# Kernel optimization log

Hardware: AMD Instinct MI355X
Metric: run time of the kernel (lower is better)

## Reference

```python
import jax, jax.numpy as jnp
import numpy as np

EPS = 1e-5


def _binary_act(x):
    # Forward: sign(x). Backward: piecewise-polynomial surrogate (ApproxSign STE).
    out3 = jnp.where(x < -1, -1.0,
            jnp.where(x < 0, x * x + 2.0 * x,
             jnp.where(x < 1, -x * x + 2.0 * x, 1.0)))
    return jax.lax.stop_gradient(jnp.sign(x) - out3) + out3


def _binarize_weights(w):
    # Per-output-channel scaling factor (detached), forward = scale*sign(w),
    # backward flows through clamp(w, -1, 1) (STE).
    scale = jax.lax.stop_gradient(jnp.mean(jnp.abs(w), axis=(1, 2, 3), keepdims=True))
    clipped = jnp.clip(w, -1.0, 1.0)
    return jax.lax.stop_gradient(scale * jnp.sign(w) - clipped) + clipped


def setup_inputs() -> dict:
    key = jax.random.key(0)
    kx, kw = jax.random.split(key)
    B, Cin, Cout, H, W = 32, 128, 128, 56, 56
    x = jax.random.normal(kx, (B, Cin, H, W), dtype=jnp.float32)
    # HardBinaryConv: weight = rand(n)*0.001 permuted then reshaped -> just random in [0, 0.001)
    w = jax.random.uniform(kw, (Cout, Cin, 3, 3), dtype=jnp.float32) * 0.001
    return {
        "x": x,
        "bias0": jnp.zeros((Cin,), jnp.float32),   # move0 LearnableBias
        "w": w,                                     # HardBinaryConv latent weights
        "gamma": jnp.ones((Cout,), jnp.float32),    # BN weight
        "beta": jnp.zeros((Cout,), jnp.float32),    # BN bias
        "bias1": jnp.zeros((Cout,), jnp.float32),   # move1
        "alpha": jnp.full((Cout,), 0.25, jnp.float32),  # PReLU per-channel
        "bias2": jnp.zeros((Cout,), jnp.float32),   # move2
    }


def reference(x, bias0, w, gamma, beta, bias1, alpha, bias2):
    def pc(v):  # per-channel broadcast (1, C, 1, 1)
        return v[None, :, None, None]

    residual = x
    out = x + pc(bias0)                     # move0
    out = _binary_act(out)                  # binary activation
    bw = _binarize_weights(w)               # {-scale, +scale} weights
    y = jax.lax.conv_general_dilated(
        out, bw, window_strides=(1, 1), padding=((1, 1), (1, 1)),
        dimension_numbers=("NCHW", "OIHW", "NCHW"))
    # BatchNorm2d (training mode: biased batch statistics over N,H,W)
    mean = jnp.mean(y, axis=(0, 2, 3), keepdims=True)
    var = jnp.mean(jnp.square(y - mean), axis=(0, 2, 3), keepdims=True)
    y = (y - mean) * jax.lax.rsqrt(var + EPS) * pc(gamma) + pc(beta)
    y = y + residual
    y = y + pc(bias1)                       # move1
    y = jnp.where(y >= 0, y, pc(alpha) * y)  # PReLU
    y = y + pc(bias2)                       # move2
    return y
```

## Files before the change

### kernel.cpp

```cpp
#include <hip/hip_runtime.h>
#include <stdint.h>

#define NB 32
#define NC 128
#define NH 56
#define NW 56
#define NHW_ (NH * NW)
#define NPIX (NB * NHW_)
#define NO 128
#define NK 1152
#define NSTRIP 14
#define NSLOT (NB * NSTRIP)

typedef unsigned long long u64;

__global__ __launch_bounds__(256) void pack_act(const float* __restrict__ x,
                                                const float* __restrict__ bias0,
                                                u64* __restrict__ packA) {
    int p = blockIdx.x * 256 + threadIdx.x;
    if (p >= NPIX) return;
    int n = p / NHW_;
    int rem = p - n * NHW_;
    const float* xb = x + (size_t)n * NC * NHW_ + rem;
    u64 w0 = 0, w1 = 0;
#pragma unroll 8
    for (int c = 0; c < 64; ++c)
        w0 |= (u64)((xb[(size_t)c * NHW_] + bias0[c]) > 0.f) << c;
#pragma unroll 8
    for (int c = 0; c < 64; ++c)
        w1 |= (u64)((xb[(size_t)(c + 64) * NHW_] + bias0[c + 64]) > 0.f) << c;
    packA[(size_t)p * 2]     = w0;
    packA[(size_t)p * 2 + 1] = w1;
}

__global__ __launch_bounds__(64) void pack_wgt(const float* __restrict__ w,
                                               u64* __restrict__ packW,
                                               float* __restrict__ scaleW,
                                               int* __restrict__ corrW) {
    __shared__ u64 sb[18];
    int o = blockIdx.x;
    int t = threadIdx.x;
    const float* wo = w + (size_t)o * NK;
    float s = 0.f;
    for (int i = t; i < NK; i += 64) s += fabsf(wo[i]);
    for (int off = 32; off; off >>= 1) s += __shfl_down(s, off);
    if (t == 0) scaleW[o] = s / (float)NK;
    if (t < 18) {
        int tap = t >> 1;
        int j   = t & 1;
        u64 bits = 0;
        for (int cc = 0; cc < 64; ++cc) {
            int c = j * 64 + cc;
            bits |= (u64)(wo[c * 9 + tap] > 0.f) << cc;
        }
        packW[(size_t)o * 18 + t] = bits;
        sb[t] = bits;
    }
    __syncthreads();
    if (t == 0) {
        int cv[9];
#pragma unroll
        for (int tap = 0; tap < 9; ++tap)
            cv[tap] = NC - 2 * (__popcll(sb[2 * tap]) + __popcll(sb[2 * tap + 1]));
        int* cw = corrW + o * 8;
        cw[0] = cv[0] + cv[3] + cv[6];
        cw[1] = cv[2] + cv[5] + cv[8];
        cw[2] = cv[0] + cv[1] + cv[2];
        cw[3] = cv[6] + cv[7] + cv[8];
        cw[4] = cv[0];
        cw[5] = cv[2];
        cw[6] = cv[6];
        cw[7] = cv[8];
    }
}

__global__ __launch_bounds__(256, 3) void conv_bin(const u64* __restrict__ packA,
                                                   const u64* __restrict__ packW,
                                                   const int* __restrict__ corrW,
                                                   short* __restrict__ yI,
                                                   int* __restrict__ sumP,
                                                   int* __restrict__ sqP) {
    __shared__ u64 lw[32 * 18];
    __shared__ int lc[32 * 8];

    int bid = blockIdx.x;
    int n = bid / (NSTRIP * 4);
    int rem = bid - n * (NSTRIP * 4);
    int strip = rem >> 2;
    int cg = rem & 3;
    int obase = cg * 32;
    int h0 = strip * 4;

    for (int i = threadIdx.x; i < 32 * 18; i += 256) lw[i] = packW[(size_t)obase * 18 + i];
    if (threadIdx.x < 32 * 8) lc[threadIdx.x] = corrW[obase * 8 + threadIdx.x];

    int wv = threadIdx.x >> 6, lane = threadIdx.x & 63;
    bool act = lane < NW;
    bool top = (strip == 0), bot = (strip == NSTRIP - 1);

    u64 a[6][3][2];
    bool cvv[3];
    cvv[0] = act && (lane >= 1);
    cvv[1] = act;
    cvv[2] = act && (lane + 1 < NW);
#pragma unroll
    for (int r = 0; r < 6; ++r) {
        int hi = h0 - 1 + r;
        bool rvv = (hi >= 0) && (hi < NH);
        int hc = hi < 0 ? 0 : (hi >= NH ? NH - 1 : hi);
#pragma unroll
        for (int c = 0; c < 3; ++c) {
            int wi = lane - 1 + c;
            int wc = wi < 0 ? 0 : (wi >= NW ? NW - 1 : wi);
            ulonglong2 q = *reinterpret_cast<const ulonglong2*>(
                packA + ((size_t)n * NHW_ + (size_t)hc * NW + wc) * 2);
            bool v = rvv && cvv[c];
            a[r][c][0] = v ? q.x : 0;
            a[r][c][1] = v ? q.y : 0;
        }
    }
    __syncthreads();

    bool isL = (lane == 0), isR = (lane == NW - 1);
    short* ybase = yI + (size_t)n * NO * NHW_ + (size_t)h0 * NW + lane;
    int sl = n * NSTRIP + strip;

    for (int oo = 0; oo < 8; ++oo) {
        int lo = (wv << 3) + oo;
        int o = obase + lo;
        const u64* wp = &lw[lo * 18];
        int pc0 = 0, pc1 = 0, pc2 = 0, pc3 = 0;
#pragma unroll
        for (int kh = 0; kh < 3; ++kh) {
#pragma unroll
            for (int kw = 0; kw < 3; ++kw) {
                u64 w0 = wp[(kh * 3 + kw) * 2];
                u64 w1 = wp[(kh * 3 + kw) * 2 + 1];
                pc0 += __popcll(a[0 + kh][kw][0] ^ w0) + __popcll(a[0 + kh][kw][1] ^ w1);
                pc1 += __popcll(a[1 + kh][kw][0] ^ w0) + __popcll(a[1 + kh][kw][1] ^ w1);
                pc2 += __popcll(a[2 + kh][kw][0] ^ w0) + __popcll(a[2 + kh][kw][1] ^ w1);
                pc3 += __popcll(a[3 + kh][kw][0] ^ w0) + __popcll(a[3 + kh][kw][1] ^ w1);
            }
        }
        const int* cw = &lc[lo * 8];
        int corrcol = isL ? cw[0] : (isR ? cw[1] : 0);
        int base = NK - corrcol;
        int d0 = base - 2 * pc0;
        int d1 = base - 2 * pc1;
        int d2 = base - 2 * pc2;
        int d3 = base - 2 * pc3;
        if (top) d0 -= cw[2] - (isL ? cw[4] : (isR ? cw[5] : 0));
        if (bot) d3 -= cw[3] - (isL ? cw[6] : (isR ? cw[7] : 0));
        if (act) {
            short* yp = ybase + (size_t)o * NHW_;
            yp[0]      = (short)d0;
            yp[NW]     = (short)d1;
            yp[2 * NW] = (short)d2;
            yp[3 * NW] = (short)d3;
        }
        int s = act ? (d0 + d1 + d2 + d3) : 0;
        int q = act ? (d0 * d0 + d1 * d1 + d2 * d2 + d3 * d3) : 0;
#pragma unroll
        for (int off = 32; off; off >>= 1) {
            s += __shfl_down(s, off);
            q += __shfl_down(q, off);
        }
        if (lane == 0) {
            sumP[o * NSLOT + sl] = s;
            sqP[o * NSLOT + sl]  = q;
        }
    }
}

__global__ __launch_bounds__(64) void bn_coef2(const int* __restrict__ sumP,
                                               const int* __restrict__ sqP,
                                               const float* __restrict__ scaleW,
                                               const float* __restrict__ gamma,
                                               const float* __restrict__ beta,
                                               const float* __restrict__ bias1,
                                               float* __restrict__ coefA,
                                               float* __restrict__ coefB) {
    int o = blockIdx.x;
    int t = threadIdx.x;
    long long s = 0, q = 0;
    for (int i = t; i < NSLOT; i += 64) {
        s += sumP[o * NSLOT + i];
        q += sqP[o * NSLOT + i];
    }
#pragma unroll
    for (int off = 32; off; off >>= 1) {
        s += __shfl_down(s, off);
        q += __shfl_down(q, off);
    }
    if (t == 0) {
        double cnt = (double)NPIX;
        double mean = (double)s / cnt;
        double var = (double)q / cnt - mean * mean;
        if (var < 0.0) var = 0.0;
        float sc = scaleW[o];
        float rs = rsqrtf((float)((double)sc * (double)sc * var) + 1e-5f);
        float g = gamma[o];
        coefA[o] = sc * g * rs;
        coefB[o] = beta[o] - (float)((double)sc * mean) * g * rs + bias1[o];
    }
}

__global__ __launch_bounds__(256) void final_store(const short* __restrict__ yI,
                                                   const float* __restrict__ x,
                                                   const float* __restrict__ coefA,
                                                   const float* __restrict__ coefB,
                                                   const float* __restrict__ alpha,
                                                   const float* __restrict__ bias2,
                                                   float* __restrict__ out) {
    const size_t ngroups = (size_t)NB * NO * NHW_ / 8;
    for (size_t g = (size_t)blockIdx.x * blockDim.x + threadIdx.x; g < ngroups;
         g += (size_t)gridDim.x * blockDim.x) {
        size_t i = g * 8;
        int o = (int)((i / NHW_) % NO);
        float a = coefA[o], bb = coefB[o], al = alpha[o], b2 = bias2[o];
        int4 yv = *reinterpret_cast<const int4*>(yI + i);
        float4 x0 = *reinterpret_cast<const float4*>(x + i);
        float4 x1 = *reinterpret_cast<const float4*>(x + i + 4);
        int q[4] = {yv.x, yv.y, yv.z, yv.w};
        float xs[8] = {x0.x, x0.y, x0.z, x0.w, x1.x, x1.y, x1.z, x1.w};
        float r[8];
#pragma unroll
        for (int j = 0; j < 4; ++j) {
            float lo = (float)(short)(q[j] & 0xffff);
            float hi = (float)(q[j] >> 16);
            float t0 = fmaf(a, lo, bb) + xs[2 * j];
            float t1 = fmaf(a, hi, bb) + xs[2 * j + 1];
            t0 = t0 >= 0.f ? t0 : al * t0;
            t1 = t1 >= 0.f ? t1 : al * t1;
            r[2 * j]     = t0 + b2;
            r[2 * j + 1] = t1 + b2;
        }
        float4 o0 = {r[0], r[1], r[2], r[3]};
        float4 o1 = {r[4], r[5], r[6], r[7]};
        *reinterpret_cast<float4*>(out + i)     = o0;
        *reinterpret_cast<float4*>(out + i + 4) = o1;
    }
}

__device__ inline void load_nbhd(const u64* __restrict__ packA, int n, int h,
                                 int wcol, bool act, u64 a[9][2], unsigned* vmask) {
    unsigned m = 0;
#pragma unroll
    for (int kh = 0; kh < 3; ++kh) {
        int hi = h + kh - 1;
        bool vh = (hi >= 0) && (hi < NH);
#pragma unroll
        for (int kw = 0; kw < 3; ++kw) {
            int wi = wcol + kw - 1;
            int t = kh * 3 + kw;
            bool v = act && vh && (wi >= 0) && (wi < NW);
            int hc = hi < 0 ? 0 : (hi >= NH ? NH - 1 : hi);
            int wc = wi < 0 ? 0 : (wi >= NW ? NW - 1 : wi);
            size_t idx = ((size_t)n * NHW_ + (size_t)hc * NW + wc) * 2;
            u64 q0 = packA[idx], q1 = packA[idx + 1];
            a[t][0] = v ? q0 : 0;
            a[t][1] = v ? q1 : 0;
            m |= (unsigned)v << t;
        }
    }
    *vmask = m;
}

__global__ __launch_bounds__(256) void conv_stats_atomic(const u64* __restrict__ packA,
                                                         const u64* __restrict__ packW,
                                                         int* __restrict__ sumI,
                                                         u64* __restrict__ sumsqI) {
    __shared__ u64 lw[NO * 18];
    for (int i = threadIdx.x; i < NO * 18; i += 256) lw[i] = packW[i];
    int nh = blockIdx.x;
    int n = nh / NH, h = nh - n * NH;
    int wave = threadIdx.x >> 6, lane = threadIdx.x & 63;
    bool act = lane < NW;
    u64 a[9][2]; unsigned vm;
    load_nbhd(packA, n, h, lane, act, a, &vm);
    __syncthreads();
    for (int oo = 0; oo < 32; ++oo) {
        int o = (wave << 5) + oo;
        int dot = 0;
#pragma unroll
        for (int t = 0; t < 9; ++t) {
            int pc = __popcll(a[t][0] ^ lw[(o * 9 + t) * 2]) +
                     __popcll(a[t][1] ^ lw[(o * 9 + t) * 2 + 1]);
            dot += ((vm >> t) & 1) ? (NC - 2 * pc) : 0;
        }
        int s = dot, sq = dot * dot;
        for (int off = 32; off; off >>= 1) {
            s  += __shfl_down(s, off);
            sq += __shfl_down(sq, off);
        }
        if (lane == 0) {
            atomicAdd(&sumI[o], s);
            atomicAdd(&sumsqI[o], (u64)(unsigned)sq);
        }
    }
}

__global__ __launch_bounds__(128) void bn_coef(const int* __restrict__ sumP,
                                               const u64* __restrict__ sqP,
                                               const float* __restrict__ scaleW,
                                               const float* __restrict__ gamma,
                                               const float* __restrict__ beta,
                                               const float* __restrict__ bias1,
                                               float* __restrict__ coefA,
                                               float* __restrict__ coefB) {
    int o = threadIdx.x;
    double cnt = (double)NPIX;
    double mean = (double)sumP[o] / cnt;
    double var = (double)sqP[o] / cnt - mean * mean;
    if (var < 0.0) var = 0.0;
    float sc = scaleW[o];
    float rs = rsqrtf((float)((double)sc * (double)sc * var) + 1e-5f);
    float g = gamma[o];
    coefA[o] = sc * g * rs;
    coefB[o] = beta[o] - (float)((double)sc * mean) * g * rs + bias1[o];
}

__global__ __launch_bounds__(256) void final_recompute(const u64* __restrict__ packA,
                                                       const u64* __restrict__ packW,
                                                       const float* __restrict__ coefA,
                                                       const float* __restrict__ coefB,
                                                       const float* __restrict__ alpha,
                                                       const float* __restrict__ bias2,
                                                       const float* __restrict__ x,
                                                       float* __restrict__ out) {
    __shared__ u64 lw[NO * 18];
    for (int i = threadIdx.x; i < NO * 18; i += 256) lw[i] = packW[i];
    int nh = blockIdx.x;
    int n = nh / NH, h = nh - n * NH;
    int wave = threadIdx.x >> 6, lane = threadIdx.x & 63;
    bool act = lane < NW;
    u64 a[9][2]; unsigned vm;
    load_nbhd(packA, n, h, lane, act, a, &vm);
    __syncthreads();
    for (int oo = 0; oo < 32; ++oo) {
        int o = (wave << 5) + oo;
        int dot = 0;
#pragma unroll
        for (int t = 0; t < 9; ++t) {
            int pc = __popcll(a[t][0] ^ lw[(o * 9 + t) * 2]) +
                     __popcll(a[t][1] ^ lw[(o * 9 + t) * 2 + 1]);
            dot += ((vm >> t) & 1) ? (NC - 2 * pc) : 0;
        }
        if (act) {
            size_t idx = ((size_t)n * NO + o) * NHW_ + (size_t)h * NW + lane;
            float t = fmaf(coefA[o], (float)dot, coefB[o]) + x[idx];
            t = t >= 0.f ? t : alpha[o] * t;
            out[idx] = t + bias2[o];
        }
    }
}

extern "C" void kernel_launch(void* const* d_in, const int* in_sizes, int n_in,
                              void* d_out, int out_size, void* d_ws, size_t ws_size,
                              hipStream_t stream) {
    (void)in_sizes; (void)n_in; (void)out_size;
    const float* x     = (const float*)d_in[0];
    const float* bias0 = (const float*)d_in[1];
    const float* w     = (const float*)d_in[2];
    const float* gamma = (const float*)d_in[3];
    const float* beta  = (const float*)d_in[4];
    const float* bias1 = (const float*)d_in[5];
    const float* alpha = (const float*)d_in[6];
    const float* bias2 = (const float*)d_in[7];
    float* out = (float*)d_out;
    char* ws = (char*)d_ws;

    u64*   packA  = (u64*)ws;
    u64*   packW  = (u64*)(ws + 1605632);
    int*   corrW  = (int*)(ws + 1624064);
    float* scaleW = (float*)(ws + 1628160);
    float* coefA  = (float*)(ws + 1628672);
    float* coefB  = (float*)(ws + 1629184);
    int*   sumI   = (int*)(ws + 1629696);
    u64*   sqI    = (u64*)(ws + 1630208);
    int*   sumP   = (int*)(ws + 1631232);
    int*   sqP    = (int*)(ws + 1860608);
    short* yI     = (short*)(ws + 2089984);
    bool store = ws_size >= (size_t)2089984 + (size_t)NB * NO * NHW_ * 2;

    pack_act<<<NPIX / 256, 256, 0, stream>>>(x, bias0, packA);
    pack_wgt<<<NO, 64, 0, stream>>>(w, packW, scaleW, corrW);

    if (store) {
        conv_bin<<<NB * NSTRIP * 4, 256, 0, stream>>>(packA, packW, corrW, yI, sumP, sqP);
        bn_coef2<<<NO, 64, 0, stream>>>(sumP, sqP, scaleW, gamma, beta, bias1, coefA, coefB);
        final_store<<<2048, 256, 0, stream>>>(yI, x, coefA, coefB, alpha, bias2, out);
    } else {
        hipMemsetAsync(sumI, 0, 512 + 1024, stream);
        conv_stats_atomic<<<NB * NH, 256, 0, stream>>>(packA, packW, sumI, sqI);
        bn_coef<<<1, NO, 0, stream>>>(sumI, sqI, scaleW, gamma, beta, bias1, coefA, coefB);
        final_recompute<<<NB * NH, 256, 0, stream>>>(packA, packW, coefA, coefB, alpha, bias2, x, out);
    }
}
```

Before: 93.34 us.

## Use zero-padded packed activations and halve conv block size

Packed activations are written into a zero-padded buffer (58x66 per image), so the conv kernel loads its neighbourhood without clamping or validity masks. The conv kernel now runs 128-thread blocks, each wave handling 16 output channels instead of 8. The recompute fallback is rebuilt as a templated conv_bin variant. This removes branch and select work in the load phase, at the cost of an extra memset of the padded buffer and slightly more pack_act writes.

```diff
diff --git a/kernel.cpp b/kernel.cpp
--- a/kernel.cpp
+++ b/kernel.cpp
@@ -12,15 +12,24 @@
 #define NSTRIP 14
 #define NSLOT (NB * NSTRIP)
 
+#define PADH 58
+#define PADW 66
+#define PAD_BYTES ((size_t)NB * PADH * PADW * 2 * 8)
+
 typedef unsigned long long u64;
+
+__device__ __forceinline__ size_t pidx(int n, int h, int w) {
+    return (((size_t)n * PADH + (h + 1)) * PADW + (w + 1)) * 2;
+}
 
 __global__ __launch_bounds__(256) void pack_act(const float* __restrict__ x,
                                                 const float* __restrict__ bias0,
-                                                u64* __restrict__ packA) {
+                                                u64* __restrict__ packAp) {
     int p = blockIdx.x * 256 + threadIdx.x;
     if (p >= NPIX) return;
     int n = p / NHW_;
     int rem = p - n * NHW_;
+    int h = rem / NW, wcol = rem - h * NW;
     const float* xb = x + (size_t)n * NC * NHW_ + rem;
     u64 w0 = 0, w1 = 0;
 #pragma unroll 8
@@ -29,8 +38,9 @@
 #pragma unroll 8
     for (int c = 0; c < 64; ++c)
         w1 |= (u64)((xb[(size_t)(c + 64) * NHW_] + bias0[c + 64]) > 0.f) << c;
-    packA[(size_t)p * 2]     = w0;
-    packA[(size_t)p * 2 + 1] = w1;
+    size_t idx = pidx(n, h, wcol);
+    packAp[idx]     = w0;
+    packAp[idx + 1] = w1;
 }
 
 __global__ __launch_bounds__(64) void pack_wgt(const float* __restrict__ w,
@@ -74,12 +84,14 @@
     }
 }
 
-__global__ __launch_bounds__(256, 3) void conv_bin(const u64* __restrict__ packA,
-                                                   const u64* __restrict__ packW,
-                                                   const int* __restrict__ corrW,
-                                                   short* __restrict__ yI,
-                                                   int* __restrict__ sumP,
-                                                   int* __restrict__ sqP) {
+template <int MODE>
+__global__ __launch_bounds__(128, 4) void conv_bin(
+    const u64* __restrict__ packAp, const u64* __restrict__ packW,
+    const int* __restrict__ corrW, short* __restrict__ yI,
+    int* __restrict__ sumP, int* __restrict__ sqP,
+    const float* __restrict__ coefA, const float* __restrict__ coefB,
+    const float* __restrict__ alpha, const float* __restrict__ bias2,
+    const float* __restrict__ x, float* __restrict__ out) {
     __shared__ u64 lw[32 * 18];
     __shared__ int lc[32 * 8];
 
@@ -87,60 +99,51 @@
     int n = bid / (NSTRIP * 4);
     int rem = bid - n * (NSTRIP * 4);
     int strip = rem >> 2;
-    int cg = rem & 3;
-    int obase = cg * 32;
+    int cgp = rem & 3;
+    int obase = cgp * 32;
     int h0 = strip * 4;
 
-    for (int i = threadIdx.x; i < 32 * 18; i += 256) lw[i] = packW[(size_t)obase * 18 + i];
-    if (threadIdx.x < 32 * 8) lc[threadIdx.x] = corrW[obase * 8 + threadIdx.x];
+    for (int i = threadIdx.x; i < 32 * 18; i += 128) lw[i] = packW[(size_t)obase * 18 + i];
+    for (int i = threadIdx.x; i < 32 * 8; i += 128) lc[i] = corrW[obase * 8 + i];
 
     int wv = threadIdx.x >> 6, lane = threadIdx.x & 63;
     bool act = lane < NW;
+
+    u64 a[6][3][2];
+    const u64* bp = packAp + (((size_t)n * PADH + h0) * PADW + lane) * 2;
+#pragma unroll
+    for (int r = 0; r < 6; ++r)
+#pragma unroll
+        for (int c = 0; c < 3; ++c) {
+            ulonglong2 q = *reinterpret_cast<const ulonglong2*>(bp + ((size_t)r * PADW + c) * 2);
+            a[r][c][0] = q.x;
+            a[r][c][1] = q.y;
+        }
+#pragma unroll
+    for (int r = 0; r < 6; ++r)
+#pragma unroll
+        for (int c = 0; c < 3; ++c)
+            asm volatile("" : "+v"(a[r][c][0]), "+v"(a[r][c][1]));
+    __syncthreads();
+
     bool top = (strip == 0), bot = (strip == NSTRIP - 1);
-
-    u64 a[6][3][2];
-    bool cvv[3];
-    cvv[0] = act && (lane >= 1);
-    cvv[1] = act;
-    cvv[2] = act && (lane + 1 < NW);
-#pragma unroll
-    for (int r = 0; r < 6; ++r) {
-        int hi = h0 - 1 + r;
-        bool rvv = (hi >= 0) && (hi < NH);
-        int hc = hi < 0 ? 0 : (hi >= NH ? NH - 1 : hi);
-#pragma unroll
-        for (int c = 0; c < 3; ++c) {
-            int wi = lane - 1 + c;
-            int wc = wi < 0 ? 0 : (wi >= NW ? NW - 1 : wi);
-            ulonglong2 q = *reinterpret_cast<const ulonglong2*>(
-                packA + ((size_t)n * NHW_ + (size_t)hc * NW + wc) * 2);
-            bool v = rvv && cvv[c];
-            a[r][c][0] = v ? q.x : 0;
-            a[r][c][1] = v ? q.y : 0;
-        }
-    }
-    __syncthreads();
-
     bool isL = (lane == 0), isR = (lane == NW - 1);
+    int sl = n * NSTRIP + strip;
     short* ybase = yI + (size_t)n * NO * NHW_ + (size_t)h0 * NW + lane;
-    int sl = n * NSTRIP + strip;
-
-    for (int oo = 0; oo < 8; ++oo) {
-        int lo = (wv << 3) + oo;
+
+    for (int oo = 0; oo < 16; ++oo) {
+        int lo = (wv << 4) + oo;
         int o = obase + lo;
         const u64* wp = &lw[lo * 18];
         int pc0 = 0, pc1 = 0, pc2 = 0, pc3 = 0;
 #pragma unroll
-        for (int kh = 0; kh < 3; ++kh) {
-#pragma unroll
-            for (int kw = 0; kw < 3; ++kw) {
-                u64 w0 = wp[(kh * 3 + kw) * 2];
-                u64 w1 = wp[(kh * 3 + kw) * 2 + 1];
-                pc0 += __popcll(a[0 + kh][kw][0] ^ w0) + __popcll(a[0 + kh][kw][1] ^ w1);
-                pc1 += __popcll(a[1 + kh][kw][0] ^ w0) + __popcll(a[1 + kh][kw][1] ^ w1);
-                pc2 += __popcll(a[2 + kh][kw][0] ^ w0) + __popcll(a[2 + kh][kw][1] ^ w1);
-                pc3 += __popcll(a[3 + kh][kw][0] ^ w0) + __popcll(a[3 + kh][kw][1] ^ w1);
-            }
+        for (int t = 0; t < 9; ++t) {
+            const int kh = t / 3, kw = t - 3 * (t / 3);
+            u64 w0 = wp[2 * t], w1 = wp[2 * t + 1];
+            pc0 += __popcll(a[kh][kw][0] ^ w0) + __popcll(a[kh][kw][1] ^ w1);
+            pc1 += __popcll(a[kh + 1][kw][0] ^ w0) + __popcll(a[kh + 1][kw][1] ^ w1);
+            pc2 += __popcll(a[kh + 2][kw][0] ^ w0) + __popcll(a[kh + 2][kw][1] ^ w1);
+            pc3 += __popcll(a[kh + 3][kw][0] ^ w0) + __popcll(a[kh + 3][kw][1] ^ w1);
         }
         const int* cw = &lc[lo * 8];
         int corrcol = isL ? cw[0] : (isR ? cw[1] : 0);
@@ -151,23 +154,38 @@
         int d3 = base - 2 * pc3;
         if (top) d0 -= cw[2] - (isL ? cw[4] : (isR ? cw[5] : 0));
         if (bot) d3 -= cw[3] - (isL ? cw[6] : (isR ? cw[7] : 0));
-        if (act) {
+
+        if (MODE == 0 && act) {
             short* yp = ybase + (size_t)o * NHW_;
             yp[0]      = (short)d0;
             yp[NW]     = (short)d1;
             yp[2 * NW] = (short)d2;
             yp[3 * NW] = (short)d3;
         }
-        int s = act ? (d0 + d1 + d2 + d3) : 0;
-        int q = act ? (d0 * d0 + d1 * d1 + d2 * d2 + d3 * d3) : 0;
-#pragma unroll
-        for (int off = 32; off; off >>= 1) {
-            s += __shfl_down(s, off);
-            q += __shfl_down(q, off);
-        }
-        if (lane == 0) {
-            sumP[o * NSLOT + sl] = s;
-            sqP[o * NSLOT + sl]  = q;
+        if (MODE <= 1) {
+            int s = act ? (d0 + d1 + d2 + d3) : 0;
+            int q = act ? (__mul24(d0, d0) + __mul24(d1, d1) +
+                           __mul24(d2, d2) + __mul24(d3, d3)) : 0;
+#pragma unroll
+            for (int off = 32; off; off >>= 1) {
+                s += __shfl_down(s, off);
+                q += __shfl_down(q, off);
+            }
+            if (lane == 0) {
+                sumP[o * NSLOT + sl] = s;
+                sqP[o * NSLOT + sl]  = q;
+            }
+        }
+        if (MODE == 2 && act) {
+            float ca = coefA[o], cb = coefB[o], al = alpha[o], b2 = bias2[o];
+            size_t idx = ((size_t)n * NO + o) * NHW_ + (size_t)h0 * NW + lane;
+            int dv[4] = {d0, d1, d2, d3};
+#pragma unroll
+            for (int r = 0; r < 4; ++r) {
+                float tv = fmaf(ca, (float)dv[r], cb) + x[idx + (size_t)r * NW];
+                tv = tv >= 0.f ? tv : al * tv;
+                out[idx + (size_t)r * NW] = tv + b2;
+            }
         }
     }
 }
@@ -242,119 +260,6 @@
     }
 }
 
-__device__ inline void load_nbhd(const u64* __restrict__ packA, int n, int h,
-                                 int wcol, bool act, u64 a[9][2], unsigned* vmask) {
-    unsigned m = 0;
-#pragma unroll
-    for (int kh = 0; kh < 3; ++kh) {
-        int hi = h + kh - 1;
-        bool vh = (hi >= 0) && (hi < NH);
-#pragma unroll
-        for (int kw = 0; kw < 3; ++kw) {
-            int wi = wcol + kw - 1;
-            int t = kh * 3 + kw;
-            bool v = act && vh && (wi >= 0) && (wi < NW);
-            int hc = hi < 0 ? 0 : (hi >= NH ? NH - 1 : hi);
-            int wc = wi < 0 ? 0 : (wi >= NW ? NW - 1 : wi);
-            size_t idx = ((size_t)n * NHW_ + (size_t)hc * NW + wc) * 2;
-            u64 q0 = packA[idx], q1 = packA[idx + 1];
-            a[t][0] = v ? q0 : 0;
-            a[t][1] = v ? q1 : 0;
-            m |= (unsigned)v << t;
-        }
-    }
-    *vmask = m;
-}
-
-__global__ __launch_bounds__(256) void conv_stats_atomic(const u64* __restrict__ packA,
-                                                         const u64* __restrict__ packW,
-                                                         int* __restrict__ sumI,
-                                                         u64* __restrict__ sumsqI) {
-    __shared__ u64 lw[NO * 18];
-    for (int i = threadIdx.x; i < NO * 18; i += 256) lw[i] = packW[i];
-    int nh = blockIdx.x;
-    int n = nh / NH, h = nh - n * NH;
-    int wave = threadIdx.x >> 6, lane = threadIdx.x & 63;
-    bool act = lane < NW;
-    u64 a[9][2]; unsigned vm;
-    load_nbhd(packA, n, h, lane, act, a, &vm);
-    __syncthreads();
-    for (int oo = 0; oo < 32; ++oo) {
-        int o = (wave << 5) + oo;
-        int dot = 0;
-#pragma unroll
-        for (int t = 0; t < 9; ++t) {
-            int pc = __popcll(a[t][0] ^ lw[(o * 9 + t) * 2]) +
-                     __popcll(a[t][1] ^ lw[(o * 9 + t) * 2 + 1]);
-            dot += ((vm >> t) & 1) ? (NC - 2 * pc) : 0;
-        }
-        int s = dot, sq = dot * dot;
-        for (int off = 32; off; off >>= 1) {
-            s  += __shfl_down(s, off);
-            sq += __shfl_down(sq, off);
-        }
-        if (lane == 0) {
-            atomicAdd(&sumI[o], s);
-            atomicAdd(&sumsqI[o], (u64)(unsigned)sq);
-        }
-    }
-}
-
-__global__ __launch_bounds__(128) void bn_coef(const int* __restrict__ sumP,
-                                               const u64* __restrict__ sqP,
-                                               const float* __restrict__ scaleW,
-                                               const float* __restrict__ gamma,
-                                               const float* __restrict__ beta,
-                                               const float* __restrict__ bias1,
-                                               float* __restrict__ coefA,
-                                               float* __restrict__ coefB) {
-    int o = threadIdx.x;
-    double cnt = (double)NPIX;
-    double mean = (double)sumP[o] / cnt;
-    double var = (double)sqP[o] / cnt - mean * mean;
-    if (var < 0.0) var = 0.0;
-    float sc = scaleW[o];
-    float rs = rsqrtf((float)((double)sc * (double)sc * var) + 1e-5f);
-    float g = gamma[o];
-    coefA[o] = sc * g * rs;
-    coefB[o] = beta[o] - (float)((double)sc * mean) * g * rs + bias1[o];
-}
-
-__global__ __launch_bounds__(256) void final_recompute(const u64* __restrict__ packA,
-                                                       const u64* __restrict__ packW,
-                                                       const float* __restrict__ coefA,
-                                                       const float* __restrict__ coefB,
-                                                       const float* __restrict__ alpha,
-                                                       const float* __restrict__ bias2,
-                                                       const float* __restrict__ x,
-                                                       float* __restrict__ out) {
-    __shared__ u64 lw[NO * 18];
-    for (int i = threadIdx.x; i < NO * 18; i += 256) lw[i] = packW[i];
-    int nh = blockIdx.x;
-    int n = nh / NH, h = nh - n * NH;
-    int wave = threadIdx.x >> 6, lane = threadIdx.x & 63;
-    bool act = lane < NW;
-    u64 a[9][2]; unsigned vm;
-    load_nbhd(packA, n, h, lane, act, a, &vm);
-    __syncthreads();
-    for (int oo = 0; oo < 32; ++oo) {
-        int o = (wave << 5) + oo;
-        int dot = 0;
-#pragma unroll
-        for (int t = 0; t < 9; ++t) {
-            int pc = __popcll(a[t][0] ^ lw[(o * 9 + t) * 2]) +
-                     __popcll(a[t][1] ^ lw[(o * 9 + t) * 2 + 1]);
-            dot += ((vm >> t) & 1) ? (NC - 2 * pc) : 0;
-        }
-        if (act) {
-            size_t idx = ((size_t)n * NO + o) * NHW_ + (size_t)h * NW + lane;
-            float t = fmaf(coefA[o], (float)dot, coefB[o]) + x[idx];
-            t = t >= 0.f ? t : alpha[o] * t;
-            out[idx] = t + bias2[o];
-        }
-    }
-}
-
 extern "C" void kernel_launch(void* const* d_in, const int* in_sizes, int n_in,
                               void* d_out, int out_size, void* d_ws, size_t ws_size,
                               hipStream_t stream) {
@@ -370,30 +275,34 @@
     float* out = (float*)d_out;
     char* ws = (char*)d_ws;
 
-    u64*   packA  = (u64*)ws;
-    u64*   packW  = (u64*)(ws + 1605632);
-    int*   corrW  = (int*)(ws + 1624064);
-    float* scaleW = (float*)(ws + 1628160);
-    float* coefA  = (float*)(ws + 1628672);
-    float* coefB  = (float*)(ws + 1629184);
-    int*   sumI   = (int*)(ws + 1629696);
-    u64*   sqI    = (u64*)(ws + 1630208);
-    int*   sumP   = (int*)(ws + 1631232);
-    int*   sqP    = (int*)(ws + 1860608);
-    short* yI     = (short*)(ws + 2089984);
-    bool store = ws_size >= (size_t)2089984 + (size_t)NB * NO * NHW_ * 2;
-
-    pack_act<<<NPIX / 256, 256, 0, stream>>>(x, bias0, packA);
+    u64*   packAp = (u64*)ws;
+    u64*   packW  = (u64*)(ws + 1959936);
+    int*   corrW  = (int*)(ws + 1978368);
+    float* scaleW = (float*)(ws + 1982464);
+    float* coefA  = (float*)(ws + 1982976);
+    float* coefB  = (float*)(ws + 1983488);
+    int*   sumP   = (int*)(ws + 1984000);
+    int*   sqP    = (int*)(ws + 2213376);
+    short* yI     = (short*)(ws + 2442752);
+    bool store = ws_size >= (size_t)2442752 + (size_t)NB * NO * NHW_ * 2;
+
+    hipMemsetAsync(packAp, 0, PAD_BYTES, stream);
+    pack_act<<<NPIX / 256, 256, 0, stream>>>(x, bias0, packAp);
     pack_wgt<<<NO, 64, 0, stream>>>(w, packW, scaleW, corrW);
 
     if (store) {
-        conv_bin<<<NB * NSTRIP * 4, 256, 0, stream>>>(packA, packW, corrW, yI, sumP, sqP);
+        conv_bin<0><<<NB * NSTRIP * 4, 128, 0, stream>>>(
+            packAp, packW, corrW, yI, sumP, sqP,
+            nullptr, nullptr, nullptr, nullptr, nullptr, nullptr);
         bn_coef2<<<NO, 64, 0, stream>>>(sumP, sqP, scaleW, gamma, beta, bias1, coefA, coefB);
         final_store<<<2048, 256, 0, stream>>>(yI, x, coefA, coefB, alpha, bias2, out);
     } else {
-        hipMemsetAsync(sumI, 0, 512 + 1024, stream);
-        conv_stats_atomic<<<NB * NH, 256, 0, stream>>>(packA, packW, sumI, sqI);
-        bn_coef<<<1, NO, 0, stream>>>(sumI, sqI, scaleW, gamma, beta, bias1, coefA, coefB);
-        final_recompute<<<NB * NH, 256, 0, stream>>>(packA, packW, coefA, coefB, alpha, bias2, x, out);
-    }
-}
+        conv_bin<1><<<NB * NSTRIP * 4, 128, 0, stream>>>(
+            packAp, packW, corrW, nullptr, sumP, sqP,
+            nullptr, nullptr, nullptr, nullptr, nullptr, nullptr);
+        bn_coef2<<<NO, 64, 0, stream>>>(sumP, sqP, scaleW, gamma, beta, bias1, coefA, coefB);
+        conv_bin<2><<<NB * NSTRIP * 4, 128, 0, stream>>>(
+            packAp, packW, corrW, nullptr, sumP, sqP,
+            coefA, coefB, alpha, bias2, x, out);
+    }
+}
```

Measured after the change: 109.7 us. +17.6%, slower.
